# Optimization experiments

Measured on AMD Instinct MI355X. Metric: run time of the kernel, lower is better.

Reference implementation:

```python
import jax, jax.numpy as jnp
import numpy as np
from jax import lax

PAD = (3, 3)
PAD_VALUE = -1.0
POOL_SIZE = 7
POOL_STRIDE = 2


def setup_inputs() -> dict:
    key = jax.random.key(0)
    k1, k2 = jax.random.split(key)
    B, Cin, L = 64, 64, 16384
    Cout, K = 128, 7
    I = jax.random.normal(k1, (B, Cin, L), dtype=jnp.float32)
    W = jax.random.normal(k2, (Cout, Cin, K), dtype=jnp.float32)
    # Threshold params are initialized to ones in the module (requires_grad=False)
    threshold_plus = jnp.ones((Cout,), dtype=jnp.float32)
    threshold_minus = jnp.ones((Cout,), dtype=jnp.float32)
    threshold_plus_sign = jnp.ones((Cout,), dtype=jnp.float32)
    threshold_minus_sign = jnp.ones((Cout,), dtype=jnp.float32)
    return {
        "I": I,
        "W": W,
        "threshold_plus": threshold_plus,
        "threshold_minus": threshold_minus,
        "threshold_plus_sign": threshold_plus_sign,
        "threshold_minus_sign": threshold_minus_sign,
    }


def reference(I, W, threshold_plus, threshold_minus, threshold_plus_sign, threshold_minus_sign):
    # 1) ConstantPad1d(padding=(3,3), value=-1.0)
    x = jnp.pad(I, ((0, 0), (0, 0), PAD), constant_values=PAD_VALUE)
    # 2) Binarize activations and weights via sign(), then float conv1d (no bias)
    ba = jnp.sign(x)
    bw = jnp.sign(W)
    conv = lax.conv_general_dilated(
        ba, bw,
        window_strides=(1,),
        padding="VALID",
        dimension_numbers=("NCH", "OIH", "NCH"),
    )  # [B, Cout, L]
    # 3) MaxPool1d(kernel_size=7, stride=2)
    pooled = lax.reduce_window(
        conv, -jnp.inf, lax.max,
        window_dimensions=(1, 1, POOL_SIZE),
        window_strides=(1, 1, POOL_STRIDE),
        padding="VALID",
    )  # [B, Cout, Lp]
    # 4) Per-channel Threshold (vectorized over channels; 2*c > 2*t == c > t)
    tp = threshold_plus[None, :, None]
    tm = threshold_minus[None, :, None]
    ps = threshold_plus_sign[None, :, None]
    ms = threshold_minus_sign[None, :, None]
    pos_branch = jnp.where(pooled > tp, ps, -ps)
    neg_branch = jnp.where(pooled > tm, ms, -ms)
    out = jnp.where(pooled >= 0, pos_branch, neg_branch)
    return out
```

## Files before the change

### kernel.cpp

```cpp
#include <hip/hip_runtime.h>
#include <stdint.h>

#define B_    64
#define CIN   64
#define L_IN  16384
#define COUT  128
#define K_    7
#define LPAD  3
#define LP    (L_IN + 2*LPAD)
#define LPA   16416
#define LOUT  8189
#define NTERMS 448
#define TOUT  8
#define CO_PER_BLK 16

__global__ __launch_bounds__(256) void pack_A(const float* __restrict__ I,
                                              uint64_t* __restrict__ A) {
    int b     = blockIdx.x >> 4;
    int chunk = blockIdx.x & 15;
    int t     = threadIdx.x;
    int l0    = chunk * 1024 + t * 4;
    const float* Ib = I + (size_t)b * CIN * L_IN + l0;
    uint64_t acc0 = 0, acc1 = 0, acc2 = 0, acc3 = 0;
#pragma unroll
    for (int ci = 0; ci < CIN; ++ci) {
        float4 v = *(const float4*)(Ib + (size_t)ci * L_IN);
        acc0 |= (uint64_t)(__float_as_uint(v.x) >> 31) << ci;
        acc1 |= (uint64_t)(__float_as_uint(v.y) >> 31) << ci;
        acc2 |= (uint64_t)(__float_as_uint(v.z) >> 31) << ci;
        acc3 |= (uint64_t)(__float_as_uint(v.w) >> 31) << ci;
    }
    uint64_t* Ab = A + (size_t)b * LPA + (LPAD + l0);
    Ab[0] = acc0; Ab[1] = acc1; Ab[2] = acc2; Ab[3] = acc3;
    if (chunk == 0 && t < 6) {
        int l = (t < 3) ? t : (L_IN + t);
        A[(size_t)b * LPA + l] = ~0ULL;
    }
}

__global__ __launch_bounds__(256) void pack_W(const float* __restrict__ W,
                                              uint64_t* __restrict__ Bp) {
    int idx = blockIdx.x * 256 + threadIdx.x;
    if (idx >= COUT * K_) return;
    int co = idx / K_, k = idx - co * K_;
    uint64_t acc = 0;
#pragma unroll
    for (int ci = 0; ci < CIN; ++ci) {
        uint32_t s = __float_as_uint(W[(size_t)co * CIN * K_ + ci * K_ + k]) >> 31;
        acc |= (uint64_t)s << ci;
    }
    Bp[idx] = acc;
}

__global__ __launch_bounds__(256) void bconv_pool_thresh(
    const uint64_t* __restrict__ A, const uint64_t* __restrict__ Bp,
    const float* __restrict__ tp_, const float* __restrict__ tm_,
    const float* __restrict__ ps_, const float* __restrict__ ms_,
    float* __restrict__ out)
{
    const int cg = blockIdx.x;
    const int lc = blockIdx.y;
    const int b  = blockIdx.z;
    const int t  = threadIdx.x;
    const int out0 = lc * 2048 + t * TOUT;

    const uint64_t* Ab = A + (size_t)b * LPA + 2 * out0;
    uint64_t a[2 * TOUT + 11];
#pragma unroll
    for (int j = 0; j < 2 * TOUT + 11; ++j) a[j] = Ab[j];

#pragma unroll 1
    for (int ci_ = 0; ci_ < CO_PER_BLK; ++ci_) {
        const int co = cg * CO_PER_BLK + ci_;
        const uint64_t* Bco = Bp + co * K_;
        const uint64_t w0 = Bco[0], w1 = Bco[1], w2 = Bco[2], w3 = Bco[3],
                       w4 = Bco[4], w5 = Bco[5], w6 = Bco[6];

        int s[2 * TOUT + 5];
#pragma unroll
        for (int j = 0; j < 2 * TOUT + 5; ++j) {
            int acc;
            acc  = __popcll(a[j + 0] ^ w0);
            acc += __popcll(a[j + 1] ^ w1);
            acc += __popcll(a[j + 2] ^ w2);
            acc += __popcll(a[j + 3] ^ w3);
            acc += __popcll(a[j + 4] ^ w4);
            acc += __popcll(a[j + 5] ^ w5);
            acc += __popcll(a[j + 6] ^ w6);
            s[j] = acc;
        }

        int p[TOUT + 2];
#pragma unroll
        for (int i = 0; i < TOUT + 2; ++i) p[i] = min(s[2 * i], s[2 * i + 1]);

        const float tp = tp_[co], tm = tm_[co], ps = ps_[co], ms = ms_[co];
        float* op = out + ((size_t)(b * COUT + co)) * LOUT + out0;
#pragma unroll
        for (int o = 0; o < TOUT; ++o) {
            int smin = min(min(p[o], p[o + 1]), min(p[o + 2], s[2 * o + 6]));
            float pooled = (float)(NTERMS - 2 * smin);
            float pos = pooled > tp ? ps : -ps;
            float neg = pooled > tm ? ms : -ms;
            float r   = (pooled >= 0.0f) ? pos : neg;
            if (out0 + o < LOUT) op[o] = r;
        }
    }
}

extern "C" void kernel_launch(void* const* d_in, const int* in_sizes, int n_in,
                              void* d_out, int out_size, void* d_ws, size_t ws_size,
                              hipStream_t stream) {
    const float* I  = (const float*)d_in[0];
    const float* W  = (const float*)d_in[1];
    const float* tp = (const float*)d_in[2];
    const float* tm = (const float*)d_in[3];
    const float* ps = (const float*)d_in[4];
    const float* ms = (const float*)d_in[5];
    float* out = (float*)d_out;

    uint64_t* A  = (uint64_t*)d_ws;
    uint64_t* Bp = (uint64_t*)((char*)d_ws + (size_t)B_ * LPA * sizeof(uint64_t));

    hipLaunchKernelGGL(pack_A, dim3(B_ * 16), dim3(256), 0, stream, I, A);
    hipLaunchKernelGGL(pack_W, dim3((COUT * K_ + 255) / 256), dim3(256), 0, stream, W, Bp);
    hipLaunchKernelGGL(bconv_pool_thresh, dim3(8, 4, B_), dim3(256), 0, stream,
                       A, Bp, tp, tm, ps, ms, out);
}
```

Baseline: 603.6 us.

## Pack activations via LDS ballot transpose, precompute integer thresholds, vectorize loads

Rewrites the activation packing to stage a 64x32 tile in LDS and build the 64-bit sign masks with wave ballots, so global reads are coalesced across channels. Weight packing now also turns the float thresholds into integer popcount thresholds and stores them with the sign bit patterns in one per-channel record. The main kernel applies the threshold with integer compares and writes raw bit patterns. It also clamps the last tile instead of guarding each store, loads the activation window as 128-bit vectors, and unrolls the channel loop by two. The tail clamp makes the last thread rewrite overlapping outputs, and the integer threshold conversion has to match the float compare semantics exactly.

Result: no change. 603.5 us (-0.0%).

```diff
diff --git a/kernel.cpp b/kernel.cpp
--- a/kernel.cpp
+++ b/kernel.cpp
@@ -6,75 +6,102 @@
 #define L_IN  16384
 #define COUT  128
 #define K_    7
-#define LPAD  3
-#define LP    (L_IN + 2*LPAD)
 #define LPA   16416
 #define LOUT  8189
-#define NTERMS 448
 #define TOUT  8
 #define CO_PER_BLK 16
+#define REC_W 16
 
-__global__ __launch_bounds__(256) void pack_A(const float* __restrict__ I,
-                                              uint64_t* __restrict__ A) {
-    int b     = blockIdx.x >> 4;
-    int chunk = blockIdx.x & 15;
-    int t     = threadIdx.x;
-    int l0    = chunk * 1024 + t * 4;
-    const float* Ib = I + (size_t)b * CIN * L_IN + l0;
-    uint64_t acc0 = 0, acc1 = 0, acc2 = 0, acc3 = 0;
+__global__ __launch_bounds__(256) void pack_A2(const float* __restrict__ I,
+                                               uint64_t* __restrict__ A) {
+    __shared__ uint32_t lds[4][64 * 33];
+    const int b  = blockIdx.y;
+    const int ct = blockIdx.x;
+    const int t  = threadIdx.x;
+    const int wv = t >> 6, ln = t & 63;
+    const int col0 = ct * 128 + wv * 32;
+    uint32_t* ldsw = lds[wv];
+
+    const int r0 = ln >> 3, cq = ln & 7;
+    const uint32_t* Ibase = (const uint32_t*)(I + (size_t)b * CIN * L_IN);
 #pragma unroll
-    for (int ci = 0; ci < CIN; ++ci) {
-        float4 v = *(const float4*)(Ib + (size_t)ci * L_IN);
-        acc0 |= (uint64_t)(__float_as_uint(v.x) >> 31) << ci;
-        acc1 |= (uint64_t)(__float_as_uint(v.y) >> 31) << ci;
-        acc2 |= (uint64_t)(__float_as_uint(v.z) >> 31) << ci;
-        acc3 |= (uint64_t)(__float_as_uint(v.w) >> 31) << ci;
+    for (int p = 0; p < 8; ++p) {
+        int row = p * 8 + r0;
+        uint4 v = *(const uint4*)(Ibase + (size_t)row * L_IN + col0 + cq * 4);
+        int base = row * 33 + cq * 4;
+        ldsw[base + 0] = v.x; ldsw[base + 1] = v.y;
+        ldsw[base + 2] = v.z; ldsw[base + 3] = v.w;
     }
-    uint64_t* Ab = A + (size_t)b * LPA + (LPAD + l0);
-    Ab[0] = acc0; Ab[1] = acc1; Ab[2] = acc2; Ab[3] = acc3;
-    if (chunk == 0 && t < 6) {
-        int l = (t < 3) ? t : (L_IN + t);
-        A[(size_t)b * LPA + l] = ~0ULL;
+    __syncthreads();
+
+    uint32_t accL = 0, accH = 0;
+#pragma unroll
+    for (int c = 0; c < 32; ++c) {
+        uint32_t u = ldsw[ln * 33 + c];
+        unsigned long long m = __ballot((int)(u >> 31));
+        if (ln == c) { accL = (uint32_t)m; accH = (uint32_t)(m >> 32); }
     }
+    if (ln < 32) {
+        uint64_t w = ((uint64_t)accH << 32) | accL;
+        A[(size_t)b * LPA + 3 + col0 + ln] = w;
+    }
+    if (ct == 0 && t < 6)
+        A[(size_t)b * LPA + (t < 3 ? t : L_IN + t)] = ~0ULL;
 }
 
-__global__ __launch_bounds__(256) void pack_W(const float* __restrict__ W,
-                                              uint64_t* __restrict__ Bp) {
-    int idx = blockIdx.x * 256 + threadIdx.x;
-    if (idx >= COUT * K_) return;
-    int co = idx / K_, k = idx - co * K_;
-    uint64_t acc = 0;
+__global__ __launch_bounds__(128) void pack_W2(const float* __restrict__ W,
+                                               const float* __restrict__ tp_,
+                                               const float* __restrict__ tm_,
+                                               const float* __restrict__ ps_,
+                                               const float* __restrict__ ms_,
+                                               uint64_t* __restrict__ Rp) {
+    int co = threadIdx.x;
+    if (co >= COUT) return;
+    uint64_t* rec = Rp + (size_t)co * REC_W;
 #pragma unroll
-    for (int ci = 0; ci < CIN; ++ci) {
-        uint32_t s = __float_as_uint(W[(size_t)co * CIN * K_ + ci * K_ + k]) >> 31;
-        acc |= (uint64_t)s << ci;
+    for (int k = 0; k < K_; ++k) {
+        uint64_t acc = 0;
+        for (int ci = 0; ci < CIN; ++ci) {
+            uint32_t s = __float_as_uint(W[(size_t)co * CIN * K_ + ci * K_ + k]) >> 31;
+            acc |= (uint64_t)s << ci;
+        }
+        rec[k] = acc;
     }
-    Bp[idx] = acc;
+    int itp = (int)ceilf((448.0f - tp_[co]) * 0.5f) - 1;
+    int itm = (int)ceilf((448.0f - tm_[co]) * 0.5f) - 1;
+    rec[7] = (uint64_t)(uint32_t)itp | ((uint64_t)(uint32_t)itm << 32);
+    rec[8] = (uint64_t)__float_as_uint(ps_[co]) |
+             ((uint64_t)__float_as_uint(ms_[co]) << 32);
 }
 
-__global__ __launch_bounds__(256) void bconv_pool_thresh(
-    const uint64_t* __restrict__ A, const uint64_t* __restrict__ Bp,
-    const float* __restrict__ tp_, const float* __restrict__ tm_,
-    const float* __restrict__ ps_, const float* __restrict__ ms_,
-    float* __restrict__ out)
+__global__ __launch_bounds__(256, 4) void bconv2(
+    const uint64_t* __restrict__ A, const uint64_t* __restrict__ Rp,
+    uint32_t* __restrict__ out)
 {
     const int cg = blockIdx.x;
     const int lc = blockIdx.y;
     const int b  = blockIdx.z;
     const int t  = threadIdx.x;
-    const int out0 = lc * 2048 + t * TOUT;
+    int out0 = lc * 2048 + t * TOUT;
+    if (out0 > LOUT - TOUT) out0 = LOUT - TOUT;
 
-    const uint64_t* Ab = A + (size_t)b * LPA + 2 * out0;
-    uint64_t a[2 * TOUT + 11];
+    const ulonglong2* Ab2 = (const ulonglong2*)(A + (size_t)b * LPA + 2 * out0);
+    uint64_t a[27];
 #pragma unroll
-    for (int j = 0; j < 2 * TOUT + 11; ++j) a[j] = Ab[j];
+    for (int j = 0; j < 13; ++j) { ulonglong2 v = Ab2[j]; a[2*j] = v.x; a[2*j+1] = v.y; }
+    a[26] = ((const uint64_t*)Ab2)[26];
 
-#pragma unroll 1
+    uint32_t* op = out + ((size_t)(b * COUT + cg * CO_PER_BLK)) * LOUT + out0;
+
+#pragma unroll 2
     for (int ci_ = 0; ci_ < CO_PER_BLK; ++ci_) {
-        const int co = cg * CO_PER_BLK + ci_;
-        const uint64_t* Bco = Bp + co * K_;
-        const uint64_t w0 = Bco[0], w1 = Bco[1], w2 = Bco[2], w3 = Bco[3],
-                       w4 = Bco[4], w5 = Bco[5], w6 = Bco[6];
+        const uint64_t* rec = Rp + (size_t)(cg * CO_PER_BLK + ci_) * REC_W;
+        const uint64_t w0 = rec[0], w1 = rec[1], w2 = rec[2], w3 = rec[3],
+                       w4 = rec[4], w5 = rec[5], w6 = rec[6];
+        const uint64_t thr = rec[7], sgn = rec[8];
+        const int itp = (int)(uint32_t)thr, itm = (int)(uint32_t)(thr >> 32);
+        const uint32_t psb = (uint32_t)sgn,  msb = (uint32_t)(sgn >> 32);
+        const uint32_t npsb = psb ^ 0x80000000u, nmsb = msb ^ 0x80000000u;
 
         int s[2 * TOUT + 5];
 #pragma unroll
@@ -94,17 +121,14 @@
 #pragma unroll
         for (int i = 0; i < TOUT + 2; ++i) p[i] = min(s[2 * i], s[2 * i + 1]);
 
-        const float tp = tp_[co], tm = tm_[co], ps = ps_[co], ms = ms_[co];
-        float* op = out + ((size_t)(b * COUT + co)) * LOUT + out0;
 #pragma unroll
         for (int o = 0; o < TOUT; ++o) {
             int smin = min(min(p[o], p[o + 1]), min(p[o + 2], s[2 * o + 6]));
-            float pooled = (float)(NTERMS - 2 * smin);
-            float pos = pooled > tp ? ps : -ps;
-            float neg = pooled > tm ? ms : -ms;
-            float r   = (pooled >= 0.0f) ? pos : neg;
-            if (out0 + o < LOUT) op[o] = r;
+            uint32_t pos = (smin <= itp) ? psb : npsb;
+            uint32_t neg = (smin <= itm) ? msb : nmsb;
+            op[o] = (smin <= 224) ? pos : neg;
         }
+        op += LOUT;
     }
 }
 
@@ -117,13 +141,12 @@
     const float* tm = (const float*)d_in[3];
     const float* ps = (const float*)d_in[4];
     const float* ms = (const float*)d_in[5];
-    float* out = (float*)d_out;
+    uint32_t* out = (uint32_t*)d_out;
 
-    uint64_t* A  = (uint64_t*)d_ws;
-    uint64_t* Bp = (uint64_t*)((char*)d_ws + (size_t)B_ * LPA * sizeof(uint64_t));
+    uint64_t* Rp = (uint64_t*)d_ws;
+    uint64_t* A  = (uint64_t*)((char*)d_ws + COUT * REC_W * sizeof(uint64_t));
 
-    hipLaunchKernelGGL(pack_A, dim3(B_ * 16), dim3(256), 0, stream, I, A);
-    hipLaunchKernelGGL(pack_W, dim3((COUT * K_ + 255) / 256), dim3(256), 0, stream, W, Bp);
-    hipLaunchKernelGGL(bconv_pool_thresh, dim3(8, 4, B_), dim3(256), 0, stream,
-                       A, Bp, tp, tm, ps, ms, out);
+    hipLaunchKernelGGL(pack_W2, dim3(1), dim3(128), 0, stream, W, tp, tm, ps, ms, Rp);
+    hipLaunchKernelGGL(pack_A2, dim3(128, B_), dim3(256), 0, stream, I, A);
+    hipLaunchKernelGGL(bconv2, dim3(8, 4, B_), dim3(256), 0, stream, A, Rp, out);
 }
```
